# Kernel tuning notes

Hardware: AMD Instinct MI355X
Metric: run time of the kernel (lower is better)

Reference implementation:

```python
import jax, jax.numpy as jnp
import numpy as np

IN, H, B = 1024, 1024, 8192


def _uniform(key, shape, stdv):
    return jax.random.uniform(key, shape, jnp.float32, -stdv, stdv)


def setup_inputs() -> dict:
    key = jax.random.key(0)
    ks = jax.random.split(key, 20)
    stdv = 1.0 / np.sqrt(H)
    inp = {
        "x": jax.random.normal(ks[0], (B, IN), jnp.float32),
        "h": jax.random.normal(ks[1], (B, H), jnp.float32),
        "c": jax.random.normal(ks[2], (B, H), jnp.float32),
        # fused input->gates weight [IN, 4H] (gate order: I, F, G, O) and bias [4H]
        "Wi": _uniform(ks[3], (IN, 4 * H), stdv),
        "bi": _uniform(ks[4], (4 * H,), stdv),
        # fused hidden->gates weight [H, 4H] and bias [4H]
        "Wh": _uniform(ks[5], (H, 4 * H), stdv),
        "bh": _uniform(ks[6], (4 * H,), stdv),
    }
    return inp


def reference(x, h, c, Wi, bi, Wh, bh):
    # Two fused GEMMs replacing the 8 separate nn.Linear calls (same math).
    gates = x @ Wi + bi + h @ Wh + bh  # [B, 4H]
    gI, gF, gG, gO = jnp.split(gates, 4, axis=-1)
    I = jax.nn.sigmoid(gI)
    F = jax.nn.sigmoid(gF)
    G = jnp.tanh(gG)   # nlF = Tanh
    O = jax.nn.sigmoid(gO)
    c_ = F * c + I * G
    h_ = O * jnp.tanh(c_)  # nlF2 = Tanh
    return (h_, c_)
```

## Files before the change

kernel.cpp:

```cpp
#include <hip/hip_runtime.h>
#include <stdint.h>

#define IN_DIM 1024
#define H_DIM  1024
#define BATCH  8192
#define KDIM   2048
#define NDIM   4096
#define BM     128
#define BN     256
#define BK     32
#define NT     (KDIM / BK)

typedef __bf16 bf16x8 __attribute__((ext_vector_type(8)));
typedef float  f32x4  __attribute__((ext_vector_type(4)));
typedef unsigned int u32;

static __device__ __forceinline__ unsigned short f2bf(float f) {
  u32 u = __builtin_bit_cast(u32, f);
  u += 0x7FFFu + ((u >> 16) & 1u);
  return (unsigned short)(u >> 16);
}

static __device__ __forceinline__ float sigm(float x) {
  return 1.0f / (1.0f + __expf(-x));
}
static __device__ __forceinline__ float tanh_fast(float x) {
  float e = __expf(-2.0f * fabsf(x));
  float t = (1.0f - e) / (1.0f + e);
  return copysignf(t, x);
}

__global__ void prep_all(const float* __restrict__ x, const float* __restrict__ h,
                         const float* __restrict__ Wi, const float* __restrict__ Wh,
                         const float* __restrict__ bi, const float* __restrict__ bh,
                         unsigned short* __restrict__ A,
                         unsigned short* __restrict__ Bt,
                         float* __restrict__ bias) {
  __shared__ float tile[32][33];
  const int b = blockIdx.x;
  const int t = threadIdx.x;

  if (b < 2048) {
    const int total = BATCH * KDIM / 4;
    for (int i = b * 256 + t; i < total; i += 2048 * 256) {
      int bb = i >> 9;
      int k = (i & 511) << 2;
      const float* src = (k < IN_DIM) ? (x + (size_t)bb * IN_DIM + k)
                                      : (h + (size_t)bb * H_DIM + (k - IN_DIM));
      float4 v = *reinterpret_cast<const float4*>(src);
      ushort4 o;
      o.x = f2bf(v.x); o.y = f2bf(v.y); o.z = f2bf(v.z); o.w = f2bf(v.w);
      *reinterpret_cast<ushort4*>(A + (size_t)bb * KDIM + k) = o;
    }
  } else if (b < 10240) {
    int bb = b - 2048;
    int k0 = (bb & 63) * 32;
    int c0 = (bb >> 6) * 32;
    int tx = t & 31;
    int ty = t >> 5;
    const float* src = (k0 < IN_DIM) ? (Wi + (size_t)k0 * NDIM)
                                     : (Wh + (size_t)(k0 - IN_DIM) * NDIM);
    for (int i = 0; i < 4; i++) {
      int r = ty + 8 * i;
      tile[r][tx] = src[(size_t)r * NDIM + c0 + tx];
    }
    __syncthreads();
    int g = c0 >> 10;
    int ubase = c0 & 1023;
    for (int i = 0; i < 4; i++) {
      int cc = ty + 8 * i;
      int u = ubase + cc;
      int j = ((u >> 4) << 6) + (g << 4) + (u & 15);
      Bt[(size_t)j * KDIM + k0 + tx] = f2bf(tile[tx][cc]);
    }
  } else {
    int j = (b - 10240) * 256 + t;
    int u = ((j >> 6) << 4) + (j & 15);
    int g = (j >> 4) & 3;
    int c = (g << 10) + u;
    bias[j] = bi[c] + bh[c];
  }
}

static __device__ __forceinline__ void gload_lds16(const void* g, void* l) {
  __builtin_amdgcn_global_load_lds(
      (const __attribute__((address_space(1))) u32*)g,
      (__attribute__((address_space(3))) u32*)l, 16, 0, 0);
}

#define MFMA __builtin_amdgcn_mfma_f32_16x16x32_bf16
#define SGB  __builtin_amdgcn_sched_group_barrier

__launch_bounds__(256, 2)
__global__ void lstm_gemm(const unsigned short* __restrict__ A,
                          const unsigned short* __restrict__ Bt,
                          const float* __restrict__ bias,
                          const float* __restrict__ Cin,
                          float* __restrict__ Hout,
                          float* __restrict__ Cout) {
  __shared__ __align__(16) char smem[49152];

  const int t  = threadIdx.x;
  const int l  = t & 63;
  const int w  = t >> 6;
  const int lane16 = l & 15;
  const int kg = l >> 4;
  const int wc = w;

  int bid = blockIdx.x;
  int swz = (bid & 7) * 128 + (bid >> 3);
  int tile_m = swz >> 4;
  int tile_n = swz & 15;
  int brow = tile_m * BM;
  int bRowB = tile_n * BN;

  const int cth = (l & 3) ^ ((l >> 3) & 3);
  const int srow = w * 16 + (l >> 2);
  const unsigned short* aq0 = A + (size_t)(brow + srow) * KDIM + cth * 8;
  const unsigned short* aq1 = aq0 + (size_t)64 * KDIM;
  const unsigned short* bq0 = Bt + (size_t)(bRowB + srow) * KDIM + cth * 8;
  const unsigned short* bq1 = bq0 + (size_t)64 * KDIM;
  const unsigned short* bq2 = bq0 + (size_t)128 * KDIM;
  const unsigned short* bq3 = bq0 + (size_t)192 * KDIM;

#define GL(gp, loff) gload_lds16((gp), smem + (loff) + w * 1024 + l * 16)

  const int rsw = ((kg ^ ((lane16 >> 1) & 3)) << 4);
  char* vRA = smem + lane16 * 64 + rsw;
  char* vRB = smem + 16384 + wc * 4096 + lane16 * 64 + rsw;

  f32x4 acc[8][4];
#pragma unroll
  for (int m = 0; m < 8; m++)
#pragma unroll
    for (int n = 0; n < 4; n++) acc[m][n] = (f32x4){0.f, 0.f, 0.f, 0.f};

  GL(bq0, 16384);          GL(bq1, 16384 + 4096);
  GL(bq2, 16384 + 8192);   GL(bq3, 16384 + 12288);
  GL(aq0, 0);              GL(aq1, 4096);
  GL(bq0 + 32, 32768);         GL(bq1 + 32, 32768 + 4096);
  GL(bq2 + 32, 32768 + 8192);  GL(bq3 + 32, 32768 + 12288);
  asm volatile("s_waitcnt vmcnt(4)" ::: "memory");
  __builtin_amdgcn_s_barrier();
  __builtin_amdgcn_sched_barrier(0);
  GL(aq0 + 32, 8192);      GL(aq1 + 32, 8192 + 4096);

  bf16x8 afrA[4], afrB[4], bfrX[2], bfrY[2];
#pragma unroll
  for (int mm = 0; mm < 4; mm++)
    afrA[mm] = *(const bf16x8*)(vRA + mm * 1024);
#pragma unroll
  for (int nn = 0; nn < 2; nn++)
    bfrX[nn] = *(const bf16x8*)(vRB + nn * 1024);
  aq0 += 64; aq1 += 64; bq0 += 64; bq1 += 64; bq2 += 64; bq3 += 64;

#define BODY(P)                                                              \
  {                                                                          \
        \
    __builtin_amdgcn_s_setprio(1);                                           \
    _Pragma("unroll") for (int nn = 0; nn < 2; nn++)                         \
      bfrY[nn] = *(const bf16x8*)(vRB + (P)*16384 + (2+nn)*1024);            \
    _Pragma("unroll") for (int mm = 0; mm < 4; mm++)                         \
      _Pragma("unroll") for (int nn = 0; nn < 2; nn++)                       \
        acc[mm][nn] = MFMA(afrA[mm], bfrX[nn], acc[mm][nn], 0, 0, 0);        \
    SGB(0x100, 1, 0); SGB(0x8, 4, 0);                                        \
    SGB(0x100, 1, 0); SGB(0x8, 4, 0);                                        \
    __builtin_amdgcn_s_setprio(0);                                           \
    __builtin_amdgcn_s_barrier();                                 \
    __builtin_amdgcn_sched_barrier(0);                                       \
                                             \
    GL(bq0, 16384 + (P)*16384);                                              \
    GL(bq1, 16384 + (P)*16384 + 4096);                                       \
    GL(bq2, 16384 + (P)*16384 + 8192);                                       \
    GL(bq3, 16384 + (P)*16384 + 12288);                                      \
        \
    __builtin_amdgcn_s_setprio(1);                                           \
    _Pragma("unroll") for (int mm = 0; mm < 4; mm++)                         \
      afrB[mm] = *(const bf16x8*)(vRA + (P)*8192 + (4+mm)*1024);             \
    _Pragma("unroll") for (int mm = 0; mm < 4; mm++)                         \
      _Pragma("unroll") for (int nn = 2; nn < 4; nn++)                       \
        acc[mm][nn] = MFMA(afrA[mm], bfrY[nn-2], acc[mm][nn], 0, 0, 0);      \
    SGB(0x100, 1, 0); SGB(0x8, 2, 0);                                        \
    SGB(0x100, 1, 0); SGB(0x8, 2, 0);                                        \
    SGB(0x100, 1, 0); SGB(0x8, 2, 0);                                        \
    SGB(0x100, 1, 0); SGB(0x8, 2, 0);                                        \
    __builtin_amdgcn_s_setprio(0);                                           \
                  \
    __builtin_amdgcn_s_setprio(1);                                           \
    _Pragma("unroll") for (int mm = 0; mm < 4; mm++)                         \
      _Pragma("unroll") for (int nn = 0; nn < 2; nn++)                       \
        acc[4+mm][nn] = MFMA(afrB[mm], bfrX[nn], acc[4+mm][nn], 0, 0, 0);    \
    __builtin_amdgcn_s_setprio(0);                                           \
                        \
    asm volatile("s_waitcnt vmcnt(4)" ::: "memory");                         \
    __builtin_amdgcn_s_barrier();                                 \
    __builtin_amdgcn_sched_barrier(0);                                       \
            \
    GL(aq0, (P)*8192);                                                       \
    GL(aq1, (P)*8192 + 4096);                                                \
          \
    __builtin_amdgcn_s_setprio(1);                                           \
    _Pragma("unroll") for (int mm = 0; mm < 4; mm++)                         \
      afrA[mm] = *(const bf16x8*)(vRA + ((P)^1)*8192 + mm*1024);             \
    _Pragma("unroll") for (int nn = 0; nn < 2; nn++)                         \
      bfrX[nn] = *(const bf16x8*)(vRB + ((P)^1)*16384 + nn*1024);            \
    _Pragma("unroll") for (int mm = 0; mm < 4; mm++)                         \
      _Pragma("unroll") for (int nn = 2; nn < 4; nn++)                       \
        acc[4+mm][nn] = MFMA(afrB[mm], bfrY[nn-2], acc[4+mm][nn], 0, 0, 0);  \
    SGB(0x100, 3, 0); SGB(0x8, 4, 0);                                        \
    SGB(0x100, 3, 0); SGB(0x8, 4, 0);                                        \
    __builtin_amdgcn_s_setprio(0);                                           \
    aq0 += 32; aq1 += 32; bq0 += 32; bq1 += 32; bq2 += 32; bq3 += 32;        \
  }

  for (int it = 0; it < NT / 2; ++it) {
    BODY(0)
    BODY(1)
  }
#undef BODY
#undef GL

  asm volatile("s_waitcnt vmcnt(0)" ::: "memory");

  const int U = tile_n * 64 + wc * 16 + lane16;
  const float* cinp = Cin + (size_t)(brow + kg * 4) * H_DIM + U;
  float cin[32];
#pragma unroll
  for (int m = 0; m < 8; m++)
#pragma unroll
    for (int r = 0; r < 4; r++)
      cin[m * 4 + r] = cinp[(size_t)(m * 16 + r) * H_DIM];
  float bv[4];
#pragma unroll
  for (int nn = 0; nn < 4; nn++)
    bv[nn] = bias[tile_n * 256 + wc * 64 + nn * 16 + lane16];

  float* hp = Hout + (size_t)(brow + kg * 4) * H_DIM + U;
  float* cp = Cout + (size_t)(brow + kg * 4) * H_DIM + U;
#pragma unroll
  for (int m = 0; m < 8; m++)
#pragma unroll
    for (int r = 0; r < 4; r++) {
      float Ig = sigm(acc[m][0][r] + bv[0]);
      float Fg = sigm(acc[m][1][r] + bv[1]);
      float Gg = tanh_fast(acc[m][2][r] + bv[2]);
      float Og = sigm(acc[m][3][r] + bv[3]);
      float cn = Fg * cin[m * 4 + r] + Ig * Gg;
      size_t off = (size_t)(m * 16 + r) * H_DIM;
      hp[off] = Og * tanh_fast(cn);
      cp[off] = cn;
    }
}

extern "C" void kernel_launch(void* const* d_in, const int* in_sizes, int n_in,
                              void* d_out, int out_size, void* d_ws, size_t ws_size,
                              hipStream_t stream) {
  const float* x  = (const float*)d_in[0];
  const float* h  = (const float*)d_in[1];
  const float* c  = (const float*)d_in[2];
  const float* Wi = (const float*)d_in[3];
  const float* bi = (const float*)d_in[4];
  const float* Wh = (const float*)d_in[5];
  const float* bh = (const float*)d_in[6];

  float* out  = (float*)d_out;
  float* Hout = out;
  float* Cout = out + (size_t)BATCH * H_DIM;

  unsigned short* Abf = (unsigned short*)d_ws;
  unsigned short* Btb = (unsigned short*)((char*)d_ws + 33554432);
  float*          bsf = (float*)((char*)d_ws + 50331648);

  prep_all<<<10256, 256, 0, stream>>>(x, h, Wi, Wh, bi, bh, Abf, Btb, bsf);
  lstm_gemm<<<1024, 256, 0, stream>>>(Abf, Btb, bsf, c, Hout, Cout);
}
```

Measured before the change: 172.6 us.

## Enlarge GEMM tile to 256x256 with 2x2 warp grid and 128x128 per-warp tiles

Doubles the block M tile from 128 to 256 and arranges the four waves as a 2x2 grid, each computing a 128x128 sub-tile with 64 accumulator fragments. This raises arithmetic intensity per LDS and global load and halves the grid to 512 blocks. The software pipeline is simplified to load all fragments once per K step, with an explicit lgkmcnt wait. In exchange, launch bounds drop to one block per CU, register pressure roughly doubles, and the per-tile fragment prefetch overlap is lost. The epilogue now reads the cell-state input inline instead of prefetching it.

```diff
diff --git a/kernel.cpp b/kernel.cpp
--- a/kernel.cpp
+++ b/kernel.cpp
@@ -6,7 +6,7 @@
 #define BATCH  8192
 #define KDIM   2048
 #define NDIM   4096
-#define BM     128
+#define BM     256
 #define BN     256
 #define BK     32
 #define NT     (KDIM / BK)
@@ -91,126 +91,105 @@
 #define MFMA __builtin_amdgcn_mfma_f32_16x16x32_bf16
 #define SGB  __builtin_amdgcn_sched_group_barrier
 
-__launch_bounds__(256, 2)
+__launch_bounds__(256, 1)
 __global__ void lstm_gemm(const unsigned short* __restrict__ A,
                           const unsigned short* __restrict__ Bt,
                           const float* __restrict__ bias,
                           const float* __restrict__ Cin,
                           float* __restrict__ Hout,
                           float* __restrict__ Cout) {
-  __shared__ __align__(16) char smem[49152];
+  __shared__ __align__(16) char smem[65536];
 
   const int t  = threadIdx.x;
   const int l  = t & 63;
   const int w  = t >> 6;
   const int lane16 = l & 15;
   const int kg = l >> 4;
-  const int wc = w;
+  const int wr = w >> 1;
+  const int wc = w & 1;
 
   int bid = blockIdx.x;
-  int swz = (bid & 7) * 128 + (bid >> 3);
-  int tile_m = swz >> 4;
+  int swz = (bid & 7) * 64 + (bid >> 3);
+  int brow = (swz >> 4) * BM;
   int tile_n = swz & 15;
-  int brow = tile_m * BM;
-  int bRowB = tile_n * BN;
-
-  const int cth = (l & 3) ^ ((l >> 3) & 3);
-  const int srow = w * 16 + (l >> 2);
-  const unsigned short* aq0 = A + (size_t)(brow + srow) * KDIM + cth * 8;
-  const unsigned short* aq1 = aq0 + (size_t)64 * KDIM;
-  const unsigned short* bq0 = Bt + (size_t)(bRowB + srow) * KDIM + cth * 8;
-  const unsigned short* bq1 = bq0 + (size_t)64 * KDIM;
-  const unsigned short* bq2 = bq0 + (size_t)128 * KDIM;
-  const unsigned short* bq3 = bq0 + (size_t)192 * KDIM;
-
-#define GL(gp, loff) gload_lds16((gp), smem + (loff) + w * 1024 + l * 16)
+  int bcol = tile_n * BN;
+
+  const int cth = (t & 3) ^ ((t >> 3) & 3);
+  const int strow = t >> 2;
+  const unsigned short* aq0 = A + (size_t)(brow +   0 + strow) * KDIM + cth * 8;
+  const unsigned short* aq1 = A + (size_t)(brow +  64 + strow) * KDIM + cth * 8;
+  const unsigned short* aq2 = A + (size_t)(brow + 128 + strow) * KDIM + cth * 8;
+  const unsigned short* aq3 = A + (size_t)(brow + 192 + strow) * KDIM + cth * 8;
+  const unsigned short* bq0 = Bt + (size_t)(bcol +   0 + strow) * KDIM + cth * 8;
+  const unsigned short* bq1 = Bt + (size_t)(bcol +  64 + strow) * KDIM + cth * 8;
+  const unsigned short* bq2 = Bt + (size_t)(bcol + 128 + strow) * KDIM + cth * 8;
+  const unsigned short* bq3 = Bt + (size_t)(bcol + 192 + strow) * KDIM + cth * 8;
+
+#define GL(gp, loff) gload_lds16((gp), smem + (loff) + t * 16)
 
   const int rsw = ((kg ^ ((lane16 >> 1) & 3)) << 4);
-  char* vRA = smem + lane16 * 64 + rsw;
-  char* vRB = smem + 16384 + wc * 4096 + lane16 * 64 + rsw;
-
-  f32x4 acc[8][4];
+  char* vA = smem + (wr * 128 + lane16) * 64 + rsw;
+  char* vB = smem + 32768 + (wc * 128 + lane16) * 64 + rsw;
+
+  f32x4 acc[8][8];
 #pragma unroll
   for (int m = 0; m < 8; m++)
 #pragma unroll
-    for (int n = 0; n < 4; n++) acc[m][n] = (f32x4){0.f, 0.f, 0.f, 0.f};
-
-  GL(bq0, 16384);          GL(bq1, 16384 + 4096);
-  GL(bq2, 16384 + 8192);   GL(bq3, 16384 + 12288);
-  GL(aq0, 0);              GL(aq1, 4096);
-  GL(bq0 + 32, 32768);         GL(bq1 + 32, 32768 + 4096);
-  GL(bq2 + 32, 32768 + 8192);  GL(bq3 + 32, 32768 + 12288);
-  asm volatile("s_waitcnt vmcnt(4)" ::: "memory");
+    for (int n = 0; n < 8; n++) acc[m][n] = (f32x4){0.f, 0.f, 0.f, 0.f};
+
+  GL(aq0, 0);      GL(aq1, 4096);      GL(aq2, 8192);      GL(aq3, 12288);
+  GL(bq0, 32768);  GL(bq1, 32768+4096);GL(bq2, 32768+8192);GL(bq3, 32768+12288);
+  GL(aq0+32, 16384);       GL(aq1+32, 16384+4096);
+  GL(aq2+32, 16384+8192);  GL(aq3+32, 16384+12288);
+  GL(bq0+32, 49152);       GL(bq1+32, 49152+4096);
+  GL(bq2+32, 49152+8192);  GL(bq3+32, 49152+12288);
+  asm volatile("s_waitcnt vmcnt(8)" ::: "memory");
   __builtin_amdgcn_s_barrier();
   __builtin_amdgcn_sched_barrier(0);
-  GL(aq0 + 32, 8192);      GL(aq1 + 32, 8192 + 4096);
-
-  bf16x8 afrA[4], afrB[4], bfrX[2], bfrY[2];
-#pragma unroll
-  for (int mm = 0; mm < 4; mm++)
-    afrA[mm] = *(const bf16x8*)(vRA + mm * 1024);
-#pragma unroll
-  for (int nn = 0; nn < 2; nn++)
-    bfrX[nn] = *(const bf16x8*)(vRB + nn * 1024);
-  aq0 += 64; aq1 += 64; bq0 += 64; bq1 += 64; bq2 += 64; bq3 += 64;
+  aq0 += 64; aq1 += 64; aq2 += 64; aq3 += 64;
+  bq0 += 64; bq1 += 64; bq2 += 64; bq3 += 64;
+
+  bf16x8 afr[8], bfr[8];
 
 #define BODY(P)                                                              \
   {                                                                          \
-        \
     __builtin_amdgcn_s_setprio(1);                                           \
-    _Pragma("unroll") for (int nn = 0; nn < 2; nn++)                         \
-      bfrY[nn] = *(const bf16x8*)(vRB + (P)*16384 + (2+nn)*1024);            \
-    _Pragma("unroll") for (int mm = 0; mm < 4; mm++)                         \
-      _Pragma("unroll") for (int nn = 0; nn < 2; nn++)                       \
-        acc[mm][nn] = MFMA(afrA[mm], bfrX[nn], acc[mm][nn], 0, 0, 0);        \
-    SGB(0x100, 1, 0); SGB(0x8, 4, 0);                                        \
-    SGB(0x100, 1, 0); SGB(0x8, 4, 0);                                        \
+    bfr[0] = *(const bf16x8*)(vB + (P)*16384);                               \
+    _Pragma("unroll") for (int mm = 0; mm < 8; mm++)                         \
+      afr[mm] = *(const bf16x8*)(vA + (P)*16384 + mm*1024);                  \
+    _Pragma("unroll") for (int nn = 1; nn < 8; nn++)                         \
+      bfr[nn] = *(const bf16x8*)(vB + (P)*16384 + nn*1024);                  \
+    _Pragma("unroll") for (int nn = 0; nn < 4; nn++)                         \
+      _Pragma("unroll") for (int mm = 0; mm < 8; mm++)                       \
+        acc[mm][nn] = MFMA(afr[mm], bfr[nn], acc[mm][nn], 0, 0, 0);          \
+    SGB(0x100, 2, 0); SGB(0x8, 4, 0);                                        \
+    SGB(0x100, 2, 0); SGB(0x8, 4, 0);                                        \
+    SGB(0x100, 2, 0); SGB(0x8, 4, 0);                                        \
+    SGB(0x100, 2, 0); SGB(0x8, 4, 0);                                        \
+    SGB(0x100, 2, 0); SGB(0x8, 4, 0);                                        \
+    SGB(0x100, 2, 0); SGB(0x8, 4, 0);                                        \
+    SGB(0x100, 2, 0); SGB(0x8, 4, 0);                                        \
+    SGB(0x100, 2, 0); SGB(0x8, 4, 0);                                        \
     __builtin_amdgcn_s_setprio(0);                                           \
+    asm volatile("s_waitcnt lgkmcnt(0)" ::: "memory");                       \
     __builtin_amdgcn_s_barrier();                                 \
     __builtin_amdgcn_sched_barrier(0);                                       \
                                              \
-    GL(bq0, 16384 + (P)*16384);                                              \
-    GL(bq1, 16384 + (P)*16384 + 4096);                                       \
-    GL(bq2, 16384 + (P)*16384 + 8192);                                       \
-    GL(bq3, 16384 + (P)*16384 + 12288);                                      \
-        \
+    GL(aq0, (P)*16384);          GL(aq1, (P)*16384 + 4096);                  \
+    GL(aq2, (P)*16384 + 8192);   GL(aq3, (P)*16384 + 12288);                 \
+    GL(bq0, 32768 + (P)*16384);         GL(bq1, 32768 + (P)*16384 + 4096);   \
+    GL(bq2, 32768 + (P)*16384 + 8192);  GL(bq3, 32768 + (P)*16384 + 12288);  \
+                                      \
     __builtin_amdgcn_s_setprio(1);                                           \
-    _Pragma("unroll") for (int mm = 0; mm < 4; mm++)                         \
-      afrB[mm] = *(const bf16x8*)(vRA + (P)*8192 + (4+mm)*1024);             \
-    _Pragma("unroll") for (int mm = 0; mm < 4; mm++)                         \
-      _Pragma("unroll") for (int nn = 2; nn < 4; nn++)                       \
-        acc[mm][nn] = MFMA(afrA[mm], bfrY[nn-2], acc[mm][nn], 0, 0, 0);      \
-    SGB(0x100, 1, 0); SGB(0x8, 2, 0);                                        \
-    SGB(0x100, 1, 0); SGB(0x8, 2, 0);                                        \
-    SGB(0x100, 1, 0); SGB(0x8, 2, 0);                                        \
-    SGB(0x100, 1, 0); SGB(0x8, 2, 0);                                        \
+    _Pragma("unroll") for (int nn = 4; nn < 8; nn++)                         \
+      _Pragma("unroll") for (int mm = 0; mm < 8; mm++)                       \
+        acc[mm][nn] = MFMA(afr[mm], bfr[nn], acc[mm][nn], 0, 0, 0);          \
     __builtin_amdgcn_s_setprio(0);                                           \
-                  \
-    __builtin_amdgcn_s_setprio(1);                                           \
-    _Pragma("unroll") for (int mm = 0; mm < 4; mm++)                         \
-      _Pragma("unroll") for (int nn = 0; nn < 2; nn++)                       \
-        acc[4+mm][nn] = MFMA(afrB[mm], bfrX[nn], acc[4+mm][nn], 0, 0, 0);    \
-    __builtin_amdgcn_s_setprio(0);                                           \
-                        \
-    asm volatile("s_waitcnt vmcnt(4)" ::: "memory");                         \
+    asm volatile("s_waitcnt vmcnt(8)" ::: "memory");                         \
     __builtin_amdgcn_s_barrier();                                 \
     __builtin_amdgcn_sched_barrier(0);                                       \
-            \
-    GL(aq0, (P)*8192);                                                       \
-    GL(aq1, (P)*8192 + 4096);                                                \
-          \
-    __builtin_amdgcn_s_setprio(1);                                           \
-    _Pragma("unroll") for (int mm = 0; mm < 4; mm++)                         \
-      afrA[mm] = *(const bf16x8*)(vRA + ((P)^1)*8192 + mm*1024);             \
-    _Pragma("unroll") for (int nn = 0; nn < 2; nn++)                         \
-      bfrX[nn] = *(const bf16x8*)(vRB + ((P)^1)*16384 + nn*1024);            \
-    _Pragma("unroll") for (int mm = 0; mm < 4; mm++)                         \
-      _Pragma("unroll") for (int nn = 2; nn < 4; nn++)                       \
-        acc[4+mm][nn] = MFMA(afrB[mm], bfrY[nn-2], acc[4+mm][nn], 0, 0, 0);  \
-    SGB(0x100, 3, 0); SGB(0x8, 4, 0);                                        \
-    SGB(0x100, 3, 0); SGB(0x8, 4, 0);                                        \
-    __builtin_amdgcn_s_setprio(0);                                           \
-    aq0 += 32; aq1 += 32; bq0 += 32; bq1 += 32; bq2 += 32; bq3 += 32;        \
+    aq0 += 32; aq1 += 32; aq2 += 32; aq3 += 32;                              \
+    bq0 += 32; bq1 += 32; bq2 += 32; bq3 += 32;                              \
   }
 
   for (int it = 0; it < NT / 2; ++it) {
@@ -222,33 +201,40 @@
 
   asm volatile("s_waitcnt vmcnt(0)" ::: "memory");
 
-  const int U = tile_n * 64 + wc * 16 + lane16;
-  const float* cinp = Cin + (size_t)(brow + kg * 4) * H_DIM + U;
-  float cin[32];
+  const int U0 = (tile_n * 4 + wc * 2) * 16 + lane16;
+  const int U1 = U0 + 16;
+  float bv[8];
+#pragma unroll
+  for (int nn = 0; nn < 8; nn++)
+    bv[nn] = bias[tile_n * 256 + wc * 128 + nn * 16 + lane16];
+
+  const int rb = brow + wr * 128 + kg * 4;
+  const float* cinp = Cin + (size_t)rb * H_DIM;
+  float* hp = Hout + (size_t)rb * H_DIM;
+  float* cp = Cout + (size_t)rb * H_DIM;
 #pragma unroll
   for (int m = 0; m < 8; m++)
 #pragma unroll
-    for (int r = 0; r < 4; r++)
-      cin[m * 4 + r] = cinp[(size_t)(m * 16 + r) * H_DIM];
-  float bv[4];
-#pragma unroll
-  for (int nn = 0; nn < 4; nn++)
-    bv[nn] = bias[tile_n * 256 + wc * 64 + nn * 16 + lane16];
-
-  float* hp = Hout + (size_t)(brow + kg * 4) * H_DIM + U;
-  float* cp = Cout + (size_t)(brow + kg * 4) * H_DIM + U;
-#pragma unroll
-  for (int m = 0; m < 8; m++)
-#pragma unroll
     for (int r = 0; r < 4; r++) {
-      float Ig = sigm(acc[m][0][r] + bv[0]);
-      float Fg = sigm(acc[m][1][r] + bv[1]);
-      float Gg = tanh_fast(acc[m][2][r] + bv[2]);
-      float Og = sigm(acc[m][3][r] + bv[3]);
-      float cn = Fg * cin[m * 4 + r] + Ig * Gg;
       size_t off = (size_t)(m * 16 + r) * H_DIM;
-      hp[off] = Og * tanh_fast(cn);
-      cp[off] = cn;
+      {
+        float Ig = sigm(acc[m][0][r] + bv[0]);
+        float Fg = sigm(acc[m][1][r] + bv[1]);
+        float Gg = tanh_fast(acc[m][2][r] + bv[2]);
+        float Og = sigm(acc[m][3][r] + bv[3]);
+        float cn = Fg * cinp[off + U0] + Ig * Gg;
+        hp[off + U0] = Og * tanh_fast(cn);
+        cp[off + U0] = cn;
+      }
+      {
+        float Ig = sigm(acc[m][4][r] + bv[4]);
+        float Fg = sigm(acc[m][5][r] + bv[5]);
+        float Gg = tanh_fast(acc[m][6][r] + bv[6]);
+        float Og = sigm(acc[m][7][r] + bv[7]);
+        float cn = Fg * cinp[off + U1] + Ig * Gg;
+        hp[off + U1] = Og * tanh_fast(cn);
+        cp[off + U1] = cn;
+      }
     }
 }
 
@@ -272,5 +258,5 @@
   float*          bsf = (float*)((char*)d_ws + 50331648);
 
   prep_all<<<10256, 256, 0, stream>>>(x, h, Wi, Wh, bi, bh, Abf, Btb, bsf);
-  lstm_gemm<<<1024, 256, 0, stream>>>(Abf, Btb, bsf, c, Hout, Cout);
-}
+  lstm_gemm<<<512, 256, 0, stream>>>(Abf, Btb, bsf, c, Hout, Cout);
+}
```

Measured after the change: 247.7 us. 43.5% more time.
